# Kernel tuning notes

Measured on AMD Instinct MI355X. Metric: run time of the kernel, lower is better.

The kernel has to match this reference:

```python
import jax, jax.numpy as jnp
import numpy as np

B, INPUT_DIM, EMB_DIM = 16384, 2048, 768
DOMAIN_NUM, MEMORY_NUM, TAU = 9, 10, 32.0


def setup_inputs() -> dict:
    key = jax.random.key(0)
    k1, k2, k3, k4, k5 = jax.random.split(key, 5)
    feature = jax.random.normal(k1, (B, INPUT_DIM), dtype=jnp.float32)
    category = jax.random.randint(k2, (B,), 0, DOMAIN_NUM, dtype=jnp.int64)
    # Linear(input_dim, emb_dim, bias=False) weights: [emb_dim, input_dim]
    W_topic = jax.random.normal(k3, (EMB_DIM, INPUT_DIM), dtype=jnp.float32) * 0.02
    W_domain = jax.random.normal(k4, (EMB_DIM, INPUT_DIM), dtype=jnp.float32) * 0.02
    # domain_num Embedding(memory_num, emb_dim) tables, stacked: [D, M, E]
    memory_tables = jax.random.normal(k5, (DOMAIN_NUM, MEMORY_NUM, EMB_DIM), dtype=jnp.float32)
    return {"feature": feature, "W_topic": W_topic, "W_domain": W_domain,
            "memory_tables": memory_tables, "category": category}


def reference(feature, W_topic, W_domain, memory_tables, category):
    eps = 1e-12
    # F.normalize(feature, p=2, dim=-1)
    norm = jnp.maximum(jnp.linalg.norm(feature, axis=-1, keepdims=True), eps)
    feat = feature / norm                                   # [B, I]
    # per-sample gather of each sample's category memory table: [B, M, E]
    mem = memory_tables[category]
    # faithful quirk: loop over domain_num indexes the BATCH dim of the stack
    D = memory_tables.shape[0]
    mems_d = mem[:D]                                        # [D, M, E]
    t = feat @ W_topic.T                                    # [B, E]
    topic_att = jax.nn.softmax(jnp.einsum('be,dme->bdm', t, mems_d) * TAU, axis=-1)
    sep = jnp.einsum('bdm,dme->bde', topic_att, mems_d)     # [B, D, E]
    dproj = feat @ W_domain.T                               # [B, E]
    domain_att = jax.nn.softmax(jnp.einsum('bde,be->bd', sep, dproj) * TAU, axis=-1)
    return domain_att[:, None, :]                           # [B, 1, D]
```

## Files before the change

### kernel.cpp

```cpp
#include <hip/hip_runtime.h>
#include <math.h>

#define TAU_F 32.0f

typedef __attribute__((ext_vector_type(8))) _Float16 half8;
typedef __attribute__((ext_vector_type(2))) __fp16 half2v;
typedef __attribute__((ext_vector_type(4))) float f32x4;

union HU { uint4 u; half8 v; };

__device__ __forceinline__ void sync_lds_only() {
    asm volatile("s_waitcnt lgkmcnt(0)" ::: "memory");
    __builtin_amdgcn_s_barrier();
}

__global__ __launch_bounds__(256) void gproj2(
    const float* __restrict__ Wt, const float* __restrict__ Wd,
    const float* __restrict__ mem, const int* __restrict__ cat,
    float* __restrict__ P)
{
    __shared__ float Ml[96 * 36];
    __shared__ float Wl[32 * 68];

    const int bid = blockIdx.x;
    const int mat = bid >> 7;
    const int ks  = (bid >> 5) & 3;
    const int ct  = bid & 31;
    const int c0  = ct * 64;
    const int tid = threadIdx.x;
    const float* __restrict__ W = mat ? Wd : Wt;

    const int tr = tid >> 4;
    const int tc = tid & 15;

    float acc[6][4];
    #pragma unroll
    for (int j = 0; j < 6; ++j)
        #pragma unroll
        for (int q = 0; q < 4; ++q) acc[j][q] = 0.f;

    for (int ch = 0; ch < 6; ++ch) {
        __syncthreads();
        #pragma unroll
        for (int p = 0; p < 3; ++p) {
            const int idx = tid + 256 * p;
            const int r   = idx >> 3;
            const int kq  = idx & 7;
            float4 v = make_float4(0.f, 0.f, 0.f, 0.f);
            if (r < 90) {
                const int d = r / 10;
                const int mrow = cat[d] * 10 + (r - d * 10);
                v = *(const float4*)(mem + (size_t)mrow * 768 + ks * 192 + ch * 32 + kq * 4);
            }
            *(float4*)(Ml + r * 36 + kq * 4) = v;
        }
        #pragma unroll
        for (int p = 0; p < 2; ++p) {
            const int idx = tid + 256 * p;
            const int e   = idx >> 4;
            const int c4  = (idx & 15) * 4;
            *(float4*)(Wl + e * 68 + c4) =
                *(const float4*)(W + (size_t)(ks * 192 + ch * 32 + e) * 2048 + c0 + c4);
        }
        __syncthreads();

        #pragma unroll
        for (int e = 0; e < 32; e += 4) {
            float4 m4[6], w4[4];
            #pragma unroll
            for (int j = 0; j < 6; ++j) m4[j] = *(const float4*)(Ml + (tr * 6 + j) * 36 + e);
            #pragma unroll
            for (int q = 0; q < 4; ++q) w4[q] = *(const float4*)(Wl + (e + q) * 68 + tc * 4);
            #pragma unroll
            for (int j = 0; j < 6; ++j) {
                const float mv[4] = {m4[j].x, m4[j].y, m4[j].z, m4[j].w};
                #pragma unroll
                for (int q = 0; q < 4; ++q) {
                    acc[j][0] = fmaf(mv[q], w4[q].x, acc[j][0]);
                    acc[j][1] = fmaf(mv[q], w4[q].y, acc[j][1]);
                    acc[j][2] = fmaf(mv[q], w4[q].z, acc[j][2]);
                    acc[j][3] = fmaf(mv[q], w4[q].w, acc[j][3]);
                }
            }
        }
    }

    #pragma unroll
    for (int j = 0; j < 6; ++j) {
        float4 v = make_float4(acc[j][0], acc[j][1], acc[j][2], acc[j][3]);
        *(float4*)(P + (size_t)ks * 393216 + (size_t)(mat * 96 + tr * 6 + j) * 2048 + c0 + tc * 4) = v;
    }
}

__global__ __launch_bounds__(256) void split_g3(
    const float* __restrict__ P, unsigned short* __restrict__ gB)
{
    const int u  = blockIdx.x * 256 + threadIdx.x;
    const int n  = u >> 8;
    const int k0 = (u & 255) * 8;

    float s[8] = {0.f, 0.f, 0.f, 0.f, 0.f, 0.f, 0.f, 0.f};
    #pragma unroll
    for (int ks = 0; ks < 4; ++ks) {
        const float4 a = *(const float4*)(P + (size_t)ks * 393216 + (size_t)n * 2048 + k0);
        const float4 b = *(const float4*)(P + (size_t)ks * 393216 + (size_t)n * 2048 + k0 + 4);
        s[0] += a.x; s[1] += a.y; s[2] += a.z; s[3] += a.w;
        s[4] += b.x; s[5] += b.y; s[6] += b.z; s[7] += b.w;
    }
    union { _Float16 h[8]; uint4 u4; } hi, lo;
    #pragma unroll
    for (int e = 0; e < 8; ++e) {
        const _Float16 h = (_Float16)s[e];
        hi.h[e] = h;
        lo.h[e] = (_Float16)(s[e] - (float)h);
    }
    const int kc = k0 >> 5;
    const int lq = (k0 >> 3) & 3;
    const int nq = n / 48;
    const int rm = n - nq * 48;
    const int j  = rm >> 4;
    const int lm = rm & 15;
    const size_t fH = (size_t)((kc * 12 + nq * 3 + j) * 2 + 0) * 512 + lq * 128 + lm * 8;
    const size_t fL = (size_t)((kc * 12 + nq * 3 + j) * 2 + 1) * 512 + lq * 128 + lm * 8;
    *(uint4*)(gB + fH) = hi.u4;
    *(uint4*)(gB + fL) = lo.u4;
}

__global__ __launch_bounds__(256, 2) void fused_mfma6(
    const float* __restrict__ feat, const unsigned short* __restrict__ gB,
    float* __restrict__ P2, float* __restrict__ ssqp)
{
    __shared__ __align__(16) unsigned short aS[4 * 64 * 44];

    const int tid = threadIdx.x;
    const int rt  = blockIdx.x >> 1;
    const int ks  = blockIdx.x & 1;
    const int row0 = rt * 64;

    const int w  = tid >> 6, l = tid & 63;
    const int lm = l & 15,  lq = l >> 4;
    const int nq = (w + blockIdx.x) & 3;
    const bool topic = (nq < 2);
    const int r8 = tid >> 2, kq = tid & 3;

    f32x4 acc[4][3];
    #pragma unroll
    for (int i = 0; i < 4; ++i)
        #pragma unroll
        for (int j = 0; j < 3; ++j) acc[i][j] = (f32x4)0.f;
    float ssq = 0.f;

    const float* fbase = feat + (size_t)(row0 + r8) * 2048 + ks * 1024 + kq * 8;
    const unsigned short* bbase = gB + (size_t)ks * 393216 + nq * 3072 + l * 8;

    float4 c0a = *(const float4*)(fbase);
    float4 c0b = *(const float4*)(fbase + 4);
    float4 c1a = *(const float4*)(fbase + 32);
    float4 c1b = *(const float4*)(fbase + 36);
    uint4 bh[3], bl[3];
    #pragma unroll
    for (int j = 0; j < 3; ++j) bh[j] = *(const uint4*)(bbase + j * 1024);
    if (topic) {
        #pragma unroll
        for (int j = 0; j < 3; ++j) bl[j] = *(const uint4*)(bbase + j * 1024 + 512);
    }

    auto cw = [&](int buf, float4 va, float4 vb) {
        const float xs[8] = {va.x, va.y, va.z, va.w, vb.x, vb.y, vb.z, vb.w};
        union { half2v h2[4]; uint4 u4; } uh, ul;
        #pragma unroll
        for (int e = 0; e < 4; ++e) {
            const float a = xs[2 * e], b = xs[2 * e + 1];
            ssq = fmaf(a, a, ssq); ssq = fmaf(b, b, ssq);
            half2v h = __builtin_amdgcn_cvt_pkrtz(a, b);
            uh.h2[e] = h;
            ul.h2[e] = __builtin_amdgcn_cvt_pkrtz(a - (float)h[0], b - (float)h[1]);
        }
        *(uint4*)(aS + (size_t)((buf * 2 + 0) * 64 + r8) * 44 + kq * 8) = uh.u4;
        *(uint4*)(aS + (size_t)((buf * 2 + 1) * 64 + r8) * 44 + kq * 8) = ul.u4;
    };

    cw(0, c0a, c0b);
    sync_lds_only();

    for (int kc = 0; kc < 32; ++kc) {
        const int kb = (kc + 1 < 32) ? kc + 1 : 31;
        uint4 bhn[3], bln[3];
        #pragma unroll
        for (int j = 0; j < 3; ++j)
            bhn[j] = *(const uint4*)(bbase + (size_t)kb * 12288 + j * 1024);
        if (topic) {
            #pragma unroll
            for (int j = 0; j < 3; ++j)
                bln[j] = *(const uint4*)(bbase + (size_t)kb * 12288 + j * 1024 + 512);
        }
        const int ka = (kc + 2 < 32) ? kc + 2 : 31;
        float4 cna = *(const float4*)(fbase + ka * 32);
        float4 cnb = *(const float4*)(fbase + ka * 32 + 4);

        if (kc < 31) cw((kc + 1) & 1, c1a, c1b);

        const int cb = kc & 1;
        half8 fh[4], fl[4];
        #pragma unroll
        for (int i = 0; i < 4; ++i) {
            HU th;
            th.u = *(const uint4*)(aS + (size_t)((cb * 2 + 0) * 64 + i * 16 + lm) * 44 + lq * 8);
            fh[i] = th.v;
        }
        if (topic) {
            #pragma unroll
            for (int i = 0; i < 4; ++i) {
                HU tl;
                tl.u = *(const uint4*)(aS + (size_t)((cb * 2 + 1) * 64 + i * 16 + lm) * 44 + lq * 8);
                fl[i] = tl.v;
            }
        }

        if (topic) {
            #pragma unroll
            for (int j = 0; j < 3; ++j) {
                HU h8, l8; h8.u = bh[j]; l8.u = bl[j];
                #pragma unroll
                for (int i = 0; i < 4; ++i) {
                    acc[i][j] = __builtin_amdgcn_mfma_f32_16x16x32_f16(fh[i], h8.v, acc[i][j], 0, 0, 0);
                    acc[i][j] = __builtin_amdgcn_mfma_f32_16x16x32_f16(fh[i], l8.v, acc[i][j], 0, 0, 0);
                    acc[i][j] = __builtin_amdgcn_mfma_f32_16x16x32_f16(fl[i], h8.v, acc[i][j], 0, 0, 0);
                }
            }
        } else {
            #pragma unroll
            for (int j = 0; j < 3; ++j) {
                HU h8; h8.u = bh[j];
                #pragma unroll
                for (int i = 0; i < 4; ++i)
                    acc[i][j] = __builtin_amdgcn_mfma_f32_16x16x32_f16(fh[i], h8.v, acc[i][j], 0, 0, 0);
            }
        }

        sync_lds_only();

        c1a = cna; c1b = cnb;
        #pragma unroll
        for (int j = 0; j < 3; ++j) bh[j] = bhn[j];
        if (topic) {
            #pragma unroll
            for (int j = 0; j < 3; ++j) bl[j] = bln[j];
        }
    }

    ssq += __shfl_xor(ssq, 1, 64);
    ssq += __shfl_xor(ssq, 2, 64);
    if (kq == 0) ssqp[(size_t)ks * 16384 + row0 + r8] = ssq;

    #pragma unroll
    for (int i = 0; i < 4; ++i)
        #pragma unroll
        for (int j = 0; j < 3; ++j)
            #pragma unroll
            for (int r = 0; r < 4; ++r)
                P2[((size_t)ks * 16384 + row0 + i * 16 + lq * 4 + r) * 192 + nq * 48 + j * 16 + lm]
                    = acc[i][j][r];
}

#define EP_SPAD 196
__global__ __launch_bounds__(256) void ep_kernel(
    const float* __restrict__ P2, const float* __restrict__ ssqp,
    float* __restrict__ out)
{
    __shared__ float sc[64 * EP_SPAD];
    const int tid  = threadIdx.x;
    const int row0 = blockIdx.x * 64;

    float4 s[12];
    #pragma unroll
    for (int p = 0; p < 12; ++p) s[p] = make_float4(0.f, 0.f, 0.f, 0.f);
    #pragma unroll
    for (int ks = 0; ks < 2; ++ks)
        #pragma unroll
        for (int p = 0; p < 12; ++p) {
            const int u   = p * 256 + tid;
            const int row = u / 48;
            const int c4  = (u - row * 48) * 4;
            const float4 v = *(const float4*)(P2 + ((size_t)ks * 16384 + row0 + row) * 192 + c4);
            s[p].x += v.x; s[p].y += v.y; s[p].z += v.z; s[p].w += v.w;
        }
    #pragma unroll
    for (int p = 0; p < 12; ++p) {
        const int u   = p * 256 + tid;
        const int row = u / 48;
        const int c4  = (u - row * 48) * 4;
        *(float4*)(sc + row * EP_SPAD + c4) = s[p];
    }
    float nsq = 0.f;
    if (tid < 64) {
        nsq = ssqp[row0 + tid] + ssqp[16384 + row0 + tid];
    }
    __syncthreads();

    if (tid < 64) {
        const int r = tid;
        const float inv = TAU_F / fmaxf(sqrtf(nsq), 1e-12f);
        const float* scr = sc + (size_t)r * EP_SPAD;
        float lg[9];
        float dmax = -1e30f;
        #pragma unroll
        for (int d = 0; d < 9; ++d) {
            const float* v = scr + d * 10;
            const float* u = scr + 96 + d * 10;
            float mx = v[0];
            #pragma unroll
            for (int m = 1; m < 10; ++m) mx = fmaxf(mx, v[m]);
            float ssum = 0.f, dot = 0.f;
            #pragma unroll
            for (int m = 0; m < 10; ++m) {
                const float p = __expf((v[m] - mx) * inv);
                ssum += p;
                dot = fmaf(p, u[m], dot);
            }
            const float lgt = (dot / ssum) * inv;
            lg[d] = lgt;
            dmax = fmaxf(dmax, lgt);
        }
        float s2 = 0.f;
        #pragma unroll
        for (int d = 0; d < 9; ++d) { const float p = __expf(lg[d] - dmax); lg[d] = p; s2 += p; }
        const float r2 = 1.0f / s2;
        #pragma unroll
        for (int d = 0; d < 9; ++d)
            out[(size_t)(row0 + r) * 9 + d] = lg[d] * r2;
    }
}

extern "C" void kernel_launch(void* const* d_in, const int* in_sizes, int n_in,
                              void* d_out, int out_size, void* d_ws, size_t ws_size,
                              hipStream_t stream) {
    const float* feature = (const float*)d_in[0];
    const float* Wt      = (const float*)d_in[1];
    const float* Wd      = (const float*)d_in[2];
    const float* mem     = (const float*)d_in[3];
    const int*   cat     = (const int*)d_in[4];

    float* P2 = (float*)d_ws;
    float* P  = (float*)d_ws;
    unsigned short* gB = (unsigned short*)((char*)d_ws + 50331648);
    float* ssqp = (float*)((char*)d_ws + 50331648 + 1572864);
    float* out = (float*)d_out;

    gproj2<<<256, 256, 0, stream>>>(Wt, Wd, mem, cat, P);
    split_g3<<<192, 256, 0, stream>>>(P, gB);
    fused_mfma6<<<512, 256, 0, stream>>>(feature, gB, P2, ssqp);
    ep_kernel<<<256, 256, 0, stream>>>(P2, ssqp, out);
}
```

Baseline: 250.1 us.

## Drop split-K and fuse softmax epilogue into the MFMA GEMM kernel

Removes the two-way split-K in the main GEMM: each block now covers all 2048 K for 64 rows, with a 64-iteration loop. The score tile is staged in LDS so the norm and the double softmax run in the same kernel, which drops the P2/ssqp workspace round trip and the separate epilogue launch. The cost is half as many blocks (256 instead of 512), so less parallelism and a longer serial K loop per block. The feature staging layout also changes to 8 threads per row covering two rows each, with a 40-element LDS stride.

```diff
diff --git a/kernel.cpp b/kernel.cpp
--- a/kernel.cpp
+++ b/kernel.cpp
@@ -126,37 +126,66 @@
     *(uint4*)(gB + fL) = lo.u4;
 }
 
-__global__ __launch_bounds__(256, 2) void fused_mfma6(
+#define SPAD 197
+
+__global__ __launch_bounds__(256, 2) void fused_mfma7(
     const float* __restrict__ feat, const unsigned short* __restrict__ gB,
-    float* __restrict__ P2, float* __restrict__ ssqp)
+    float* __restrict__ out)
 {
-    __shared__ __align__(16) unsigned short aS[4 * 64 * 44];
-
-    const int tid = threadIdx.x;
-    const int rt  = blockIdx.x >> 1;
-    const int ks  = blockIdx.x & 1;
-    const int row0 = rt * 64;
-
+    __shared__ __align__(16) char smem[50688];
+    __shared__ float ssqf[64];
+    unsigned short* aS = (unsigned short*)smem;
+    float* scores = (float*)smem;
+
+    const int tid  = threadIdx.x;
+    const int row0 = blockIdx.x * 64;
     const int w  = tid >> 6, l = tid & 63;
     const int lm = l & 15,  lq = l >> 4;
     const int nq = (w + blockIdx.x) & 3;
     const bool topic = (nq < 2);
-    const int r8 = tid >> 2, kq = tid & 3;
+
+    const int srow = tid >> 3;
+    const int skf  = (tid & 7) * 4;
 
     f32x4 acc[4][3];
     #pragma unroll
     for (int i = 0; i < 4; ++i)
         #pragma unroll
         for (int j = 0; j < 3; ++j) acc[i][j] = (f32x4)0.f;
-    float ssq = 0.f;
-
-    const float* fbase = feat + (size_t)(row0 + r8) * 2048 + ks * 1024 + kq * 8;
-    const unsigned short* bbase = gB + (size_t)ks * 393216 + nq * 3072 + l * 8;
-
-    float4 c0a = *(const float4*)(fbase);
-    float4 c0b = *(const float4*)(fbase + 4);
-    float4 c1a = *(const float4*)(fbase + 32);
-    float4 c1b = *(const float4*)(fbase + 36);
+    float ssq0 = 0.f, ssq1 = 0.f;
+
+    const float* fb0 = feat + (size_t)(row0 + srow) * 2048 + skf;
+    const float* fb1 = feat + (size_t)(row0 + 32 + srow) * 2048 + skf;
+    const unsigned short* bbase = gB + nq * 3072 + l * 8;
+
+    auto cw = [&](int buf, float4 va, float4 vb) {
+        union { half2v h2[2]; uint2 u2; } h0, l0, h1, l1;
+        ssq0 = fmaf(va.x, va.x, ssq0); ssq0 = fmaf(va.y, va.y, ssq0);
+        ssq0 = fmaf(va.z, va.z, ssq0); ssq0 = fmaf(va.w, va.w, ssq0);
+        ssq1 = fmaf(vb.x, vb.x, ssq1); ssq1 = fmaf(vb.y, vb.y, ssq1);
+        ssq1 = fmaf(vb.z, vb.z, ssq1); ssq1 = fmaf(vb.w, vb.w, ssq1);
+        half2v a01 = __builtin_amdgcn_cvt_pkrtz(va.x, va.y);
+        half2v a23 = __builtin_amdgcn_cvt_pkrtz(va.z, va.w);
+        h0.h2[0] = a01; h0.h2[1] = a23;
+        l0.h2[0] = __builtin_amdgcn_cvt_pkrtz(va.x - (float)a01[0], va.y - (float)a01[1]);
+        l0.h2[1] = __builtin_amdgcn_cvt_pkrtz(va.z - (float)a23[0], va.w - (float)a23[1]);
+        half2v b01 = __builtin_amdgcn_cvt_pkrtz(vb.x, vb.y);
+        half2v b23 = __builtin_amdgcn_cvt_pkrtz(vb.z, vb.w);
+        h1.h2[0] = b01; h1.h2[1] = b23;
+        l1.h2[0] = __builtin_amdgcn_cvt_pkrtz(vb.x - (float)b01[0], vb.y - (float)b01[1]);
+        l1.h2[1] = __builtin_amdgcn_cvt_pkrtz(vb.z - (float)b23[0], vb.w - (float)b23[1]);
+        unsigned short* pH = aS + (size_t)((buf * 2 + 0) * 64) * 40;
+        unsigned short* pL = aS + (size_t)((buf * 2 + 1) * 64) * 40;
+        *(uint2*)(pH + srow * 40 + skf)        = h0.u2;
+        *(uint2*)(pH + (srow + 32) * 40 + skf) = h1.u2;
+        *(uint2*)(pL + srow * 40 + skf)        = l0.u2;
+        *(uint2*)(pL + (srow + 32) * 40 + skf) = l1.u2;
+    };
+
+    float4 a00 = *(const float4*)(fb0);
+    float4 a01 = *(const float4*)(fb1);
+    float4 a10 = *(const float4*)(fb0 + 32);
+    float4 a11 = *(const float4*)(fb1 + 32);
     uint4 bh[3], bl[3];
     #pragma unroll
     for (int j = 0; j < 3; ++j) bh[j] = *(const uint4*)(bbase + j * 1024);
@@ -164,27 +193,11 @@
         #pragma unroll
         for (int j = 0; j < 3; ++j) bl[j] = *(const uint4*)(bbase + j * 1024 + 512);
     }
-
-    auto cw = [&](int buf, float4 va, float4 vb) {
-        const float xs[8] = {va.x, va.y, va.z, va.w, vb.x, vb.y, vb.z, vb.w};
-        union { half2v h2[4]; uint4 u4; } uh, ul;
-        #pragma unroll
-        for (int e = 0; e < 4; ++e) {
-            const float a = xs[2 * e], b = xs[2 * e + 1];
-            ssq = fmaf(a, a, ssq); ssq = fmaf(b, b, ssq);
-            half2v h = __builtin_amdgcn_cvt_pkrtz(a, b);
-            uh.h2[e] = h;
-            ul.h2[e] = __builtin_amdgcn_cvt_pkrtz(a - (float)h[0], b - (float)h[1]);
-        }
-        *(uint4*)(aS + (size_t)((buf * 2 + 0) * 64 + r8) * 44 + kq * 8) = uh.u4;
-        *(uint4*)(aS + (size_t)((buf * 2 + 1) * 64 + r8) * 44 + kq * 8) = ul.u4;
-    };
-
-    cw(0, c0a, c0b);
+    cw(0, a00, a01);
     sync_lds_only();
 
-    for (int kc = 0; kc < 32; ++kc) {
-        const int kb = (kc + 1 < 32) ? kc + 1 : 31;
+    for (int kc = 0; kc < 64; ++kc) {
+        const int kb = (kc + 1 < 64) ? kc + 1 : 63;
         uint4 bhn[3], bln[3];
         #pragma unroll
         for (int j = 0; j < 3; ++j)
@@ -194,25 +207,25 @@
             for (int j = 0; j < 3; ++j)
                 bln[j] = *(const uint4*)(bbase + (size_t)kb * 12288 + j * 1024 + 512);
         }
-        const int ka = (kc + 2 < 32) ? kc + 2 : 31;
-        float4 cna = *(const float4*)(fbase + ka * 32);
-        float4 cnb = *(const float4*)(fbase + ka * 32 + 4);
-
-        if (kc < 31) cw((kc + 1) & 1, c1a, c1b);
+        const int ka = (kc + 2 < 64) ? kc + 2 : 63;
+        float4 fa0 = *(const float4*)(fb0 + ka * 32);
+        float4 fa1 = *(const float4*)(fb1 + ka * 32);
+
+        if (kc < 63) cw((kc + 1) & 1, a10, a11);
 
         const int cb = kc & 1;
         half8 fh[4], fl[4];
         #pragma unroll
         for (int i = 0; i < 4; ++i) {
             HU th;
-            th.u = *(const uint4*)(aS + (size_t)((cb * 2 + 0) * 64 + i * 16 + lm) * 44 + lq * 8);
+            th.u = *(const uint4*)(aS + (size_t)((cb * 2 + 0) * 64 + i * 16 + lm) * 40 + lq * 8);
             fh[i] = th.v;
         }
         if (topic) {
             #pragma unroll
             for (int i = 0; i < 4; ++i) {
                 HU tl;
-                tl.u = *(const uint4*)(aS + (size_t)((cb * 2 + 1) * 64 + i * 16 + lm) * 44 + lq * 8);
+                tl.u = *(const uint4*)(aS + (size_t)((cb * 2 + 1) * 64 + i * 16 + lm) * 40 + lq * 8);
                 fl[i] = tl.v;
             }
         }
@@ -240,7 +253,7 @@
 
         sync_lds_only();
 
-        c1a = cna; c1b = cnb;
+        a10 = fa0; a11 = fa1;
         #pragma unroll
         for (int j = 0; j < 3; ++j) bh[j] = bhn[j];
         if (topic) {
@@ -249,9 +262,11 @@
         }
     }
 
-    ssq += __shfl_xor(ssq, 1, 64);
-    ssq += __shfl_xor(ssq, 2, 64);
-    if (kq == 0) ssqp[(size_t)ks * 16384 + row0 + r8] = ssq;
+    ssq0 += __shfl_xor(ssq0, 1, 64); ssq1 += __shfl_xor(ssq1, 1, 64);
+    ssq0 += __shfl_xor(ssq0, 2, 64); ssq1 += __shfl_xor(ssq1, 2, 64);
+    ssq0 += __shfl_xor(ssq0, 4, 64); ssq1 += __shfl_xor(ssq1, 4, 64);
+    if ((tid & 7) == 0) { ssqf[srow] = ssq0; ssqf[32 + srow] = ssq1; }
+    __syncthreads();
 
     #pragma unroll
     for (int i = 0; i < 4; ++i)
@@ -259,55 +274,19 @@
         for (int j = 0; j < 3; ++j)
             #pragma unroll
             for (int r = 0; r < 4; ++r)
-                P2[((size_t)ks * 16384 + row0 + i * 16 + lq * 4 + r) * 192 + nq * 48 + j * 16 + lm]
-                    = acc[i][j][r];
-}
-
-#define EP_SPAD 196
-__global__ __launch_bounds__(256) void ep_kernel(
-    const float* __restrict__ P2, const float* __restrict__ ssqp,
-    float* __restrict__ out)
-{
-    __shared__ float sc[64 * EP_SPAD];
-    const int tid  = threadIdx.x;
-    const int row0 = blockIdx.x * 64;
-
-    float4 s[12];
-    #pragma unroll
-    for (int p = 0; p < 12; ++p) s[p] = make_float4(0.f, 0.f, 0.f, 0.f);
-    #pragma unroll
-    for (int ks = 0; ks < 2; ++ks)
-        #pragma unroll
-        for (int p = 0; p < 12; ++p) {
-            const int u   = p * 256 + tid;
-            const int row = u / 48;
-            const int c4  = (u - row * 48) * 4;
-            const float4 v = *(const float4*)(P2 + ((size_t)ks * 16384 + row0 + row) * 192 + c4);
-            s[p].x += v.x; s[p].y += v.y; s[p].z += v.z; s[p].w += v.w;
-        }
-    #pragma unroll
-    for (int p = 0; p < 12; ++p) {
-        const int u   = p * 256 + tid;
-        const int row = u / 48;
-        const int c4  = (u - row * 48) * 4;
-        *(float4*)(sc + row * EP_SPAD + c4) = s[p];
-    }
-    float nsq = 0.f;
-    if (tid < 64) {
-        nsq = ssqp[row0 + tid] + ssqp[16384 + row0 + tid];
-    }
+                scores[(size_t)(i * 16 + lq * 4 + r) * SPAD + nq * 48 + j * 16 + lm] = acc[i][j][r];
     __syncthreads();
 
     if (tid < 64) {
         const int r = tid;
-        const float inv = TAU_F / fmaxf(sqrtf(nsq), 1e-12f);
-        const float* scr = sc + (size_t)r * EP_SPAD;
+        const float inv = TAU_F / fmaxf(sqrtf(ssqf[r]), 1e-12f);
+        const float* sc = scores + (size_t)r * SPAD;
         float lg[9];
         float dmax = -1e30f;
         #pragma unroll
         for (int d = 0; d < 9; ++d) {
-            const float* v = scr + d * 10;
-            const float* u = scr + 96 + d * 10;
+            const float* v = sc + d * 10;
+            const float* u = sc + 96 + d * 10;
             float mx = v[0];
             #pragma unroll
             for (int m = 1; m < 10; ++m) mx = fmaxf(mx, v[m]);
@@ -341,14 +320,11 @@
     const float* mem     = (const float*)d_in[3];
     const int*   cat     = (const int*)d_in[4];
 
-    float* P2 = (float*)d_ws;
     float* P  = (float*)d_ws;
     unsigned short* gB = (unsigned short*)((char*)d_ws + 50331648);
-    float* ssqp = (float*)((char*)d_ws + 50331648 + 1572864);
     float* out = (float*)d_out;
 
     gproj2<<<256, 256, 0, stream>>>(Wt, Wd, mem, cat, P);
     split_g3<<<192, 256, 0, stream>>>(P, gB);
-    fused_mfma6<<<512, 256, 0, stream>>>(feature, gB, P2, ssqp);
-    ep_kernel<<<256, 256, 0, stream>>>(P2, ssqp, out);
-}
+    fused_mfma7<<<256, 256, 0, stream>>>(feature, gB, out);
+}
```

Result: slower. 255.4 us (+2.1%).
